# Kernel tuning notes

Hardware: AMD Instinct MI355X
Metric: run time of the kernel (lower is better)

The kernel has to match this reference:

```python
import jax, jax.numpy as jnp
import numpy as np

N_TOKENS = 262144
D_IN = 128
D_OUT = 128
N_EXPERTS = 8


def setup_inputs() -> dict:
    key = jax.random.key(0)
    k1, k2, k3, k4 = jax.random.split(key, 4)
    x = jax.random.normal(k1, (N_TOKENS, D_IN), dtype=jnp.float32)
    split = jax.random.randint(k2, (N_TOKENS,), 0, N_EXPERTS, dtype=jnp.int64)
    # Per-expert Linear params (one "model" per unique split value).
    W = jax.random.normal(k3, (N_EXPERTS, D_IN, D_OUT), dtype=jnp.float32) / np.sqrt(D_IN)
    b = jax.random.normal(k4, (N_EXPERTS, D_OUT), dtype=jnp.float32)
    return {"x": x, "split": split, "W": W, "b": b}


def reference(x, split, W, b):
    # Original 'alone' path: gather rows per unique split value, apply
    # model[split_value], concat, then reorder via argsort of the gathered
    # indices. That composition is exactly a per-token expert apply:
    #   out[t] = x[t] @ W[split[t]] + b[split[t]]
    # Computed densely per expert (fixed shapes, jit-friendly), then select.
    y_all = jnp.einsum('nf,efg->eng', x, W) + b[:, None, :]  # [E, N, d_out]
    tok = jnp.arange(x.shape[0])
    return y_all[split, tok]  # [N, d_out]
```

## Files before the change

kernel.cpp:

```cpp
#include <hip/hip_runtime.h>


typedef __bf16 bf16x8 __attribute__((ext_vector_type(8)));
typedef unsigned short u16x8 __attribute__((ext_vector_type(8)));
typedef float f32x4 __attribute__((ext_vector_type(4)));

__device__ __forceinline__ unsigned short f2bf(float f) {
    unsigned u = __builtin_bit_cast(unsigned, f);
    u += 0x7FFFu + ((u >> 16) & 1u);
    return (unsigned short)(u >> 16);
}
__device__ __forceinline__ unsigned pack2(float a, float b) {
    return (unsigned)f2bf(a) | ((unsigned)f2bf(b) << 16);
}

__global__ void k_wt(const float* __restrict__ W, unsigned short* __restrict__ Wt) {
    __shared__ float T[16][132];
    int e = blockIdx.x >> 3;
    int g0 = (blockIdx.x & 7) << 4;
    const float* We = W + e * 128 * 128;
    #pragma unroll
    for (int i = 0; i < 2; ++i) {
        int idx = i * 256 + threadIdx.x;
        int f = idx >> 2, q = idx & 3;
        float4 v = *(const float4*)(We + f * 128 + g0 + q * 4);
        T[q * 4 + 0][f] = v.x; T[q * 4 + 1][f] = v.y;
        T[q * 4 + 2][f] = v.z; T[q * 4 + 3][f] = v.w;
    }
    __syncthreads();
    int g = threadIdx.x >> 4, fc = threadIdx.x & 15;
    u16x8 o;
    #pragma unroll
    for (int j = 0; j < 8; ++j) o[j] = f2bf(T[g][fc * 8 + j]);
    *(u16x8*)(Wt + ((e * 128 + g0 + g) * 128 + fc * 8)) = o;
}

#define NT 128

__global__ __launch_bounds__(256, 4) void k_fused(
    const float* __restrict__ x, const int* __restrict__ split,
    const float* __restrict__ bias, const unsigned short* __restrict__ Wt,
    float* __restrict__ out) {

    __shared__ unsigned short A[NT * 128];
    __shared__ int wcnt[16];
    __shared__ int startE[8], off1[8];
    __shared__ int dest[NT], trow[NT];
    __shared__ int exT[16], rbT[16], limT[16];
    __shared__ int Tn;

    const int tid = threadIdx.x;
    const int lane = tid & 63, w = tid >> 6;
    const long t0 = (long)blockIdx.x * NT;

    float4 xv[16];
    const float* xb = x + t0 * 128;
    #pragma unroll
    for (int rr = 0; rr < 16; ++rr)
        xv[rr] = *(const float4*)(xb + (rr * 256 + tid) * 4);

    int e = 255, myrank = 0;
    if (tid < NT) e = split[t0 + tid];
    const unsigned long long below = (lane == 63) ? ~0ull >> 1 : (1ull << lane) - 1;
    #pragma unroll
    for (int ee = 0; ee < 8; ++ee) {
        unsigned long long m = __ballot(e == ee);
        if (e == ee) myrank = (int)__popcll(m & below);
        if (w < 2 && lane == ee) wcnt[w * 8 + ee] = (int)__popcll(m);
    }
    __syncthreads();

    if (w == 0 && lane < 8) {
        int c0 = wcnt[lane], c1 = wcnt[8 + lane];
        int cE = c0 + c1;
        int v = cE;
        #pragma unroll
        for (int d = 1; d < 8; d <<= 1) { int t2 = __shfl_up(v, d, 64); if (lane >= d) v += t2; }
        int sE = v - cE;
        startE[lane] = sE; off1[lane] = sE + c0;
        int nt = (cE + 15) >> 4;
        int u = nt;
        #pragma unroll
        for (int d = 1; d < 8; d <<= 1) { int t2 = __shfl_up(u, d, 64); if (lane >= d) u += t2; }
        int tb = u - nt;
        for (int k = 0; k < nt; ++k) {
            exT[tb + k] = lane; rbT[tb + k] = sE + k * 16;
            int rem = cE - k * 16; limT[tb + k] = rem < 16 ? rem : 16;
        }
        if (lane == 7) Tn = u;
    }
    __syncthreads();

    if (tid < NT) {
        int s = (w == 0 ? startE[e] : off1[e]) + myrank;
        dest[tid] = s;
        trow[s] = tid;
    }
    __syncthreads();

    #pragma unroll
    for (int rr = 0; rr < 16; ++rr) {
        int c = rr * 256 + tid;
        int row = c >> 5;
        int s = dest[row];
        int fc = (c & 31) >> 1;
        int half = c & 1;
        unsigned d0 = pack2(xv[rr].x, xv[rr].y);
        unsigned d1 = pack2(xv[rr].z, xv[rr].w);
        *(uint2*)(A + s * 128 + ((fc ^ (s & 7)) << 3) + half * 4) = make_uint2(d0, d1);
    }
    __syncthreads();

    const int l15 = lane & 15, lq = lane >> 4;
    const int T = Tn;

    bf16x8 bfrag[2][4];
    float bv[2];
    int preve = -1;

    for (int tau = 0; tau < T; ++tau) {
        int ee = exT[tau], rb = rbT[tau], lim = limT[tau];
        if (ee != preve) {
            preve = ee;
            #pragma unroll
            for (int j = 0; j < 2; ++j) {
                const unsigned short* Wb = Wt + ee * 16384 + (w * 32 + j * 16 + l15) * 128;
                #pragma unroll
                for (int kk = 0; kk < 4; ++kk)
                    bfrag[j][kk] = *(const bf16x8*)(Wb + (kk * 4 + lq) * 8);
                bv[j] = bias[ee * 128 + w * 32 + j * 16 + l15];
            }
        }
        int srow = rb + l15;
        srow = srow < NT ? srow : NT - 1;
        f32x4 acc0 = {0.f, 0.f, 0.f, 0.f}, acc1 = {0.f, 0.f, 0.f, 0.f};
        #pragma unroll
        for (int kk = 0; kk < 4; ++kk) {
            int fc = kk * 4 + lq;
            bf16x8 a = *(const bf16x8*)(A + srow * 128 + ((fc ^ (srow & 7)) << 3));
            acc0 = __builtin_amdgcn_mfma_f32_16x16x32_bf16(a, bfrag[0][kk], acc0, 0, 0, 0);
            acc1 = __builtin_amdgcn_mfma_f32_16x16x32_bf16(a, bfrag[1][kk], acc1, 0, 0, 0);
        }
        #pragma unroll
        for (int r = 0; r < 4; ++r) {
            int ri = lq * 4 + r;
            if (ri < lim) {
                long o = (t0 + trow[rb + ri]) * 128 + w * 32 + l15;
                out[o]      = acc0[r] + bv[0];
                out[o + 16] = acc1[r] + bv[1];
            }
        }
    }
}

extern "C" void kernel_launch(void* const* d_in, const int* in_sizes, int n_in,
                              void* d_out, int out_size, void* d_ws, size_t ws_size,
                              hipStream_t stream) {
    const float* x     = (const float*)d_in[0];
    const int*   split = (const int*)d_in[1];
    const float* W     = (const float*)d_in[2];
    const float* bias  = (const float*)d_in[3];
    float* out = (float*)d_out;

    int n = in_sizes[1];
    unsigned short* Wt = (unsigned short*)d_ws;

    k_wt<<<64, 256, 0, stream>>>(W, Wt);
    k_fused<<<n / NT, 256, 0, stream>>>(x, split, bias, Wt, out);
}
```

Baseline: 95.67 us.

## Stage outputs in shared memory for coalesced float4 stores, process columns in halves

Results of the per-expert MFMA tiles are written into a padded shared-memory buffer indexed by original token row, then copied to global memory as contiguous float4 rows. Previously each lane scattered scalar stores to permuted token rows. To fit the staging buffer, output columns are handled in two 64-wide halves, each wave covering 16 columns, which doubles the tile loop and the weight-fragment reloads and adds barriers. Launch bounds drop to 2 blocks per SM, since shared memory grows by about 34KB. The ballot mask expression is also simplified.

```diff
diff --git a/kernel.cpp b/kernel.cpp
--- a/kernel.cpp
+++ b/kernel.cpp
@@ -36,13 +36,15 @@
 }
 
 #define NT 128
+#define OSTR 68
 
-__global__ __launch_bounds__(256, 4) void k_fused(
+__global__ __launch_bounds__(256, 2) void k_fused(
     const float* __restrict__ x, const int* __restrict__ split,
     const float* __restrict__ bias, const unsigned short* __restrict__ Wt,
     float* __restrict__ out) {
 
     __shared__ unsigned short A[NT * 128];
+    __shared__ float O[NT * OSTR];
     __shared__ int wcnt[16];
     __shared__ int startE[8], off1[8];
     __shared__ int dest[NT], trow[NT];
@@ -61,7 +63,7 @@
 
     int e = 255, myrank = 0;
     if (tid < NT) e = split[t0 + tid];
-    const unsigned long long below = (lane == 63) ? ~0ull >> 1 : (1ull << lane) - 1;
+    const unsigned long long below = (1ull << lane) - 1;
     #pragma unroll
     for (int ee = 0; ee < 8; ++ee) {
         unsigned long long m = __ballot(e == ee);
@@ -105,51 +107,54 @@
         int s = dest[row];
         int fc = (c & 31) >> 1;
         int half = c & 1;
-        unsigned d0 = pack2(xv[rr].x, xv[rr].y);
-        unsigned d1 = pack2(xv[rr].z, xv[rr].w);
-        *(uint2*)(A + s * 128 + ((fc ^ (s & 7)) << 3) + half * 4) = make_uint2(d0, d1);
+        *(uint2*)(A + s * 128 + ((fc ^ (s & 7)) << 3) + half * 4) =
+            make_uint2(pack2(xv[rr].x, xv[rr].y), pack2(xv[rr].z, xv[rr].w));
     }
     __syncthreads();
 
     const int l15 = lane & 15, lq = lane >> 4;
     const int T = Tn;
 
-    bf16x8 bfrag[2][4];
-    float bv[2];
-    int preve = -1;
-
-    for (int tau = 0; tau < T; ++tau) {
-        int ee = exT[tau], rb = rbT[tau], lim = limT[tau];
-        if (ee != preve) {
-            preve = ee;
-            #pragma unroll
-            for (int j = 0; j < 2; ++j) {
-                const unsigned short* Wb = Wt + ee * 16384 + (w * 32 + j * 16 + l15) * 128;
+    for (int h = 0; h < 2; ++h) {
+        int preve = -1;
+        bf16x8 bfrag[4];
+        float bv = 0.f;
+        for (int tau = 0; tau < T; ++tau) {
+            int ee = exT[tau], rb = rbT[tau], lim = limT[tau];
+            if (ee != preve) {
+                preve = ee;
+                const unsigned short* Wb = Wt + ee * 16384 + (h * 64 + w * 16 + l15) * 128;
                 #pragma unroll
                 for (int kk = 0; kk < 4; ++kk)
-                    bfrag[j][kk] = *(const bf16x8*)(Wb + (kk * 4 + lq) * 8);
-                bv[j] = bias[ee * 128 + w * 32 + j * 16 + l15];
+                    bfrag[kk] = *(const bf16x8*)(Wb + (kk * 4 + lq) * 8);
+                bv = bias[ee * 128 + h * 64 + w * 16 + l15];
+            }
+            int srow = rb + l15;
+            srow = srow < NT ? srow : NT - 1;
+            f32x4 acc = {0.f, 0.f, 0.f, 0.f};
+            #pragma unroll
+            for (int kk = 0; kk < 4; ++kk) {
+                int fc = kk * 4 + lq;
+                bf16x8 a = *(const bf16x8*)(A + srow * 128 + ((fc ^ (srow & 7)) << 3));
+                acc = __builtin_amdgcn_mfma_f32_16x16x32_bf16(a, bfrag[kk], acc, 0, 0, 0);
+            }
+            #pragma unroll
+            for (int r = 0; r < 4; ++r) {
+                int ri = lq * 4 + r;
+                if (ri < lim)
+                    O[trow[rb + ri] * OSTR + w * 16 + l15] = acc[r] + bv;
             }
         }
-        int srow = rb + l15;
-        srow = srow < NT ? srow : NT - 1;
-        f32x4 acc0 = {0.f, 0.f, 0.f, 0.f}, acc1 = {0.f, 0.f, 0.f, 0.f};
+        __syncthreads();
         #pragma unroll
-        for (int kk = 0; kk < 4; ++kk) {
-            int fc = kk * 4 + lq;
-            bf16x8 a = *(const bf16x8*)(A + srow * 128 + ((fc ^ (srow & 7)) << 3));
-            acc0 = __builtin_amdgcn_mfma_f32_16x16x32_bf16(a, bfrag[0][kk], acc0, 0, 0, 0);
-            acc1 = __builtin_amdgcn_mfma_f32_16x16x32_bf16(a, bfrag[1][kk], acc1, 0, 0, 0);
+        for (int j = 0; j < 8; ++j) {
+            int g4 = j * 256 + tid;
+            int row = g4 >> 4;
+            int c4 = (g4 & 15) << 2;
+            float4 v = *(const float4*)&O[row * OSTR + c4];
+            *(float4*)(out + (t0 + row) * 128 + h * 64 + c4) = v;
         }
-        #pragma unroll
-        for (int r = 0; r < 4; ++r) {
-            int ri = lq * 4 + r;
-            if (ri < lim) {
-                long o = (t0 + trow[rb + ri]) * 128 + w * 32 + l15;
-                out[o]      = acc0[r] + bv[0];
-                out[o + 16] = acc1[r] + bv[1];
-            }
-        }
+        __syncthreads();
     }
 }
 
```

After: 104.8 us. +9.5%, slower.

## Replace tile-table scheduling with per-expert loop and lighter LDS barriers

Applied to the files above, without the earlier changes.

Removes the serial single-wave prefix-scan step that built a tile schedule table, computing expert offsets directly from warp counts, which eliminates one block barrier. The compute loop now iterates over the eight experts and their row blocks directly, loading weight fragments once per expert. Barriers become an LDS-only waitcnt plus s_barrier so outstanding global loads of x are not drained, and a sched_barrier keeps those loads issued early. The weight-transpose store is also split into 32-bit writes. These barriers assume no global memory traffic needs ordering across them, which holds for this code.

```diff
diff --git a/kernel.cpp b/kernel.cpp
--- a/kernel.cpp
+++ b/kernel.cpp
@@ -2,7 +2,6 @@
 
 
 typedef __bf16 bf16x8 __attribute__((ext_vector_type(8)));
-typedef unsigned short u16x8 __attribute__((ext_vector_type(8)));
 typedef float f32x4 __attribute__((ext_vector_type(4)));
 
 __device__ __forceinline__ unsigned short f2bf(float f) {
@@ -29,10 +28,13 @@
     }
     __syncthreads();
     int g = threadIdx.x >> 4, fc = threadIdx.x & 15;
-    u16x8 o;
+    unsigned short o[8];
     #pragma unroll
     for (int j = 0; j < 8; ++j) o[j] = f2bf(T[g][fc * 8 + j]);
-    *(u16x8*)(Wt + ((e * 128 + g0 + g) * 128 + fc * 8)) = o;
+    #pragma unroll
+    for (int j = 0; j < 4; ++j)
+        ((unsigned*)(Wt + (e * 128 + g0 + g) * 128 + fc * 8))[j] =
+            (unsigned)o[2 * j] | ((unsigned)o[2 * j + 1] << 16);
 }
 
 #define NT 128
@@ -43,111 +45,101 @@
     float* __restrict__ out) {
 
     __shared__ unsigned short A[NT * 128];
-    __shared__ int wcnt[16];
-    __shared__ int startE[8], off1[8];
+    __shared__ int wcnt[2][8];
+    __shared__ int cntE[8], startE[8];
     __shared__ int dest[NT], trow[NT];
-    __shared__ int exT[16], rbT[16], limT[16];
-    __shared__ int Tn;
 
     const int tid = threadIdx.x;
     const int lane = tid & 63, w = tid >> 6;
+    const int l15 = lane & 15, lq = lane >> 4;
     const long t0 = (long)blockIdx.x * NT;
+
+    auto LBAR = [&]() {
+        asm volatile("s_waitcnt lgkmcnt(0)" ::: "memory");
+        __builtin_amdgcn_s_barrier();
+    };
 
     float4 xv[16];
     const float* xb = x + t0 * 128;
     #pragma unroll
     for (int rr = 0; rr < 16; ++rr)
         xv[rr] = *(const float4*)(xb + (rr * 256 + tid) * 4);
+    __builtin_amdgcn_sched_barrier(0);
 
-    int e = 255, myrank = 0;
+    int e = 255, rank = 0;
     if (tid < NT) e = split[t0 + tid];
-    const unsigned long long below = (lane == 63) ? ~0ull >> 1 : (1ull << lane) - 1;
+    const unsigned long long below = (1ull << lane) - 1;
     #pragma unroll
     for (int ee = 0; ee < 8; ++ee) {
         unsigned long long m = __ballot(e == ee);
-        if (e == ee) myrank = (int)__popcll(m & below);
-        if (w < 2 && lane == ee) wcnt[w * 8 + ee] = (int)__popcll(m);
+        if (e == ee) rank = (int)__popcll(m & below);
+        if (w < 2 && lane == ee) wcnt[w][ee] = (int)__popcll(m);
     }
-    __syncthreads();
-
-    if (w == 0 && lane < 8) {
-        int c0 = wcnt[lane], c1 = wcnt[8 + lane];
-        int cE = c0 + c1;
-        int v = cE;
-        #pragma unroll
-        for (int d = 1; d < 8; d <<= 1) { int t2 = __shfl_up(v, d, 64); if (lane >= d) v += t2; }
-        int sE = v - cE;
-        startE[lane] = sE; off1[lane] = sE + c0;
-        int nt = (cE + 15) >> 4;
-        int u = nt;
-        #pragma unroll
-        for (int d = 1; d < 8; d <<= 1) { int t2 = __shfl_up(u, d, 64); if (lane >= d) u += t2; }
-        int tb = u - nt;
-        for (int k = 0; k < nt; ++k) {
-            exT[tb + k] = lane; rbT[tb + k] = sE + k * 16;
-            int rem = cE - k * 16; limT[tb + k] = rem < 16 ? rem : 16;
-        }
-        if (lane == 7) Tn = u;
-    }
-    __syncthreads();
+    LBAR();
 
     if (tid < NT) {
-        int s = (w == 0 ? startE[e] : off1[e]) + myrank;
-        dest[tid] = s;
-        trow[s] = tid;
+        int s = 0;
+        #pragma unroll
+        for (int ee = 0; ee < 8; ++ee) s += (ee < e) ? (wcnt[0][ee] + wcnt[1][ee]) : 0;
+        int slot = s + (w == 1 ? wcnt[0][e] : 0) + rank;
+        dest[tid] = slot;
+        trow[slot] = tid;
     }
-    __syncthreads();
+    if (tid < 8) {
+        int s = 0;
+        #pragma unroll
+        for (int ee = 0; ee < 8; ++ee) s += (ee < tid) ? (wcnt[0][ee] + wcnt[1][ee]) : 0;
+        startE[tid] = s;
+        cntE[tid] = wcnt[0][tid] + wcnt[1][tid];
+    }
+    LBAR();
 
     #pragma unroll
     for (int rr = 0; rr < 16; ++rr) {
         int c = rr * 256 + tid;
         int row = c >> 5;
         int s = dest[row];
-        int fc = (c & 31) >> 1;
-        int half = c & 1;
-        unsigned d0 = pack2(xv[rr].x, xv[rr].y);
-        unsigned d1 = pack2(xv[rr].z, xv[rr].w);
-        *(uint2*)(A + s * 128 + ((fc ^ (s & 7)) << 3) + half * 4) = make_uint2(d0, d1);
+        int fc = (c & 31) >> 1, half = c & 1;
+        *(uint2*)(&A[s * 128 + ((fc ^ (s & 7)) << 3) + half * 4]) =
+            make_uint2(pack2(xv[rr].x, xv[rr].y), pack2(xv[rr].z, xv[rr].w));
     }
-    __syncthreads();
+    LBAR();
 
-    const int l15 = lane & 15, lq = lane >> 4;
-    const int T = Tn;
+    #pragma unroll
+    for (int ee = 0; ee < 8; ++ee) {
+        int cnt = cntE[ee];
+        if (cnt == 0) continue;
+        int st = startE[ee];
 
-    bf16x8 bfrag[2][4];
-    float bv[2];
-    int preve = -1;
-
-    for (int tau = 0; tau < T; ++tau) {
-        int ee = exT[tau], rb = rbT[tau], lim = limT[tau];
-        if (ee != preve) {
-            preve = ee;
-            #pragma unroll
-            for (int j = 0; j < 2; ++j) {
-                const unsigned short* Wb = Wt + ee * 16384 + (w * 32 + j * 16 + l15) * 128;
-                #pragma unroll
-                for (int kk = 0; kk < 4; ++kk)
-                    bfrag[j][kk] = *(const bf16x8*)(Wb + (kk * 4 + lq) * 8);
-                bv[j] = bias[ee * 128 + w * 32 + j * 16 + l15];
-            }
-        }
-        int srow = rb + l15;
-        srow = srow < NT ? srow : NT - 1;
-        f32x4 acc0 = {0.f, 0.f, 0.f, 0.f}, acc1 = {0.f, 0.f, 0.f, 0.f};
+        bf16x8 bfrag0[4], bfrag1[4];
         #pragma unroll
         for (int kk = 0; kk < 4; ++kk) {
-            int fc = kk * 4 + lq;
-            bf16x8 a = *(const bf16x8*)(A + srow * 128 + ((fc ^ (srow & 7)) << 3));
-            acc0 = __builtin_amdgcn_mfma_f32_16x16x32_bf16(a, bfrag[0][kk], acc0, 0, 0, 0);
-            acc1 = __builtin_amdgcn_mfma_f32_16x16x32_bf16(a, bfrag[1][kk], acc1, 0, 0, 0);
+            bfrag0[kk] = *(const bf16x8*)(Wt + (ee * 128 + w * 32 + l15) * 128 + kk * 32 + lq * 8);
+            bfrag1[kk] = *(const bf16x8*)(Wt + (ee * 128 + w * 32 + 16 + l15) * 128 + kk * 32 + lq * 8);
         }
-        #pragma unroll
-        for (int r = 0; r < 4; ++r) {
-            int ri = lq * 4 + r;
-            if (ri < lim) {
-                long o = (t0 + trow[rb + ri]) * 128 + w * 32 + l15;
-                out[o]      = acc0[r] + bv[0];
-                out[o + 16] = acc1[r] + bv[1];
+        float bv0 = bias[ee * 128 + w * 32 + l15];
+        float bv1 = bias[ee * 128 + w * 32 + 16 + l15];
+
+        for (int rb = st; rb < st + cnt; rb += 16) {
+            int lim = st + cnt - rb; lim = lim < 16 ? lim : 16;
+            int sr = rb + l15; sr = sr < NT ? sr : NT - 1;
+            f32x4 acc0 = {0.f, 0.f, 0.f, 0.f}, acc1 = {0.f, 0.f, 0.f, 0.f};
+            #pragma unroll
+            for (int kk = 0; kk < 4; ++kk) {
+                int fc = kk * 4 + lq;
+                bf16x8 a = *(const bf16x8*)(&A[sr * 128 + ((fc ^ (sr & 7)) << 3)]);
+                acc0 = __builtin_amdgcn_mfma_f32_16x16x32_bf16(a, bfrag0[kk], acc0, 0, 0, 0);
+                acc1 = __builtin_amdgcn_mfma_f32_16x16x32_bf16(a, bfrag1[kk], acc1, 0, 0, 0);
+            }
+            #pragma unroll
+            for (int r = 0; r < 4; ++r) {
+                int ri = lq * 4 + r;
+                if (ri < lim) {
+                    int tok = trow[rb + ri];
+                    float* o = out + (t0 + tok) * 128 + w * 32 + l15;
+                    o[0]  = acc0[r] + bv0;
+                    o[16] = acc1[r] + bv1;
+                }
             }
         }
     }
```

Measured after the change: 93.12 us. 1.03x faster.
